# Optimization experiments

Hardware: AMD Instinct MI355X
Metric: run time of the kernel (lower is better)

Reference implementation:

```python
import jax, jax.numpy as jnp
import numpy as np

DIM = 1024
K = 3
T = 32768


def setup_inputs() -> dict:
    key = jax.random.key(0)
    k1, k2 = jax.random.split(key)
    x = jax.random.normal(k1, (T, DIM), dtype=jnp.float32)
    coeffs = jax.random.normal(k2, (DIM, 2 * K + 1), dtype=jnp.float32) * 0.001
    return {"x": x, "coeffs": coeffs}


def reference(x, coeffs):
    # coeffs layout per original module: [:, 0] constant, [:, 2k-1] sin(k*x), [:, 2k] cos(k*x)
    ks = jnp.arange(1, K + 1, dtype=x.dtype)            # [K]
    ang = x[:, :, None] * ks                            # [T, D, K]
    s = jnp.sin(ang)                                    # [T, D, K]
    c = jnp.cos(ang)                                    # [T, D, K]
    c_const = coeffs[:, 0]                              # [D]
    c_sin = coeffs[:, 1::2]                             # [D, K] (indices 1,3,5)
    c_cos = coeffs[:, 2::2]                             # [D, K] (indices 2,4,6)
    correction = (c_const[None, :]
                  + jnp.einsum('tdk,dk->td', s, c_sin)
                  + jnp.einsum('tdk,dk->td', c, c_cos))
    return x + correction
```

## Files before the change

### kernel.cpp

```cpp
#include <hip/hip_runtime.h>
#include <math.h>

#define DIM   1024
#define NROWS 32768

__global__ __launch_bounds__(256) void fourier_kan_kernel(
    const float* __restrict__ x, const float* __restrict__ coeffs,
    float* __restrict__ out, int n_rows)
{
    const int tid = threadIdx.x;
    const int d0  = tid * 4;

    float cc0[4], cs1[4], cc1[4], cs2[4], cc2[4], cs3[4], cc3[4];
#pragma unroll
    for (int j = 0; j < 4; ++j) {
        const float* cp = coeffs + (size_t)(d0 + j) * 7;
        cc0[j] = cp[0];
        cs1[j] = cp[1]; cc1[j] = cp[2];
        cs2[j] = cp[3]; cc2[j] = cp[4];
        cs3[j] = cp[5]; cc3[j] = cp[6];
    }

    for (int t = blockIdx.x; t < n_rows; t += gridDim.x) {
        const size_t base = (size_t)t * DIM + d0;
        const float4 xv = *reinterpret_cast<const float4*>(x + base);
        float xin[4] = {xv.x, xv.y, xv.z, xv.w};
        float o[4];
#pragma unroll
        for (int j = 0; j < 4; ++j) {
            float s1, c1;
            __sincosf(xin[j], &s1, &c1);
            const float s2 = 2.0f * s1 * c1;
            const float c2 = 1.0f - 2.0f * s1 * s1;
            const float s3 = s2 * c1 + c2 * s1;
            const float c3 = c2 * c1 - s2 * s1;
            float corr = cc0[j];
            corr = fmaf(s1, cs1[j], corr);
            corr = fmaf(c1, cc1[j], corr);
            corr = fmaf(s2, cs2[j], corr);
            corr = fmaf(c2, cc2[j], corr);
            corr = fmaf(s3, cs3[j], corr);
            corr = fmaf(c3, cc3[j], corr);
            o[j] = xin[j] + corr;
        }
        float4 ov = {o[0], o[1], o[2], o[3]};
        *reinterpret_cast<float4*>(out + base) = ov;
    }
}

extern "C" void kernel_launch(void* const* d_in, const int* in_sizes, int n_in,
                              void* d_out, int out_size, void* d_ws, size_t ws_size,
                              hipStream_t stream) {
    const float* x      = (const float*)d_in[0];
    const float* coeffs = (const float*)d_in[1];
    float* out          = (float*)d_out;
    (void)in_sizes; (void)n_in; (void)out_size; (void)d_ws; (void)ws_size;

    const int grid = 4096;
    fourier_kan_kernel<<<grid, 256, 0, stream>>>(x, coeffs, out, NROWS);
}
```

Measured before the change: 238.7 us.

## Issue eight row loads up front per block with vector coeff loads and nontemporal stores

Replaces the grid-stride row loop with a fixed 8 rows per block, issuing all eight float4 loads before any compute so more memory requests are in flight per thread. Coefficients are now read as seven 16-byte vector loads instead of 28 scalar loads. Output uses nontemporal stores to avoid polluting cache. The grid becomes 4096 blocks each covering exactly 8 rows, so NROWS must be a multiple of RPB.

```diff
diff --git a/kernel.cpp b/kernel.cpp
--- a/kernel.cpp
+++ b/kernel.cpp
@@ -3,49 +3,60 @@
 
 #define DIM   1024
 #define NROWS 32768
+#define RPB   8
+
+typedef float v4f __attribute__((ext_vector_type(4)));
+
+__device__ __forceinline__ float fk_elem(float xin,
+    float C0, float S1, float C1, float S2, float C2, float S3, float C3)
+{
+    float s1, c1;
+    __sincosf(xin, &s1, &c1);
+    const float s2 = 2.0f * s1 * c1;
+    const float c2 = 1.0f - 2.0f * s1 * s1;
+    const float s3 = s2 * c1 + c2 * s1;
+    const float c3 = c2 * c1 - s2 * s1;
+    float corr = C0;
+    corr = fmaf(s1, S1, corr);
+    corr = fmaf(c1, C1, corr);
+    corr = fmaf(s2, S2, corr);
+    corr = fmaf(c2, C2, corr);
+    corr = fmaf(s3, S3, corr);
+    corr = fmaf(c3, C3, corr);
+    return xin + corr;
+}
 
 __global__ __launch_bounds__(256) void fourier_kan_kernel(
     const float* __restrict__ x, const float* __restrict__ coeffs,
-    float* __restrict__ out, int n_rows)
+    float* __restrict__ out)
 {
     const int tid = threadIdx.x;
-    const int d0  = tid * 4;
+    const int t0  = blockIdx.x * RPB;
 
-    float cc0[4], cs1[4], cc1[4], cs2[4], cc2[4], cs3[4], cc3[4];
-#pragma unroll
-    for (int j = 0; j < 4; ++j) {
-        const float* cp = coeffs + (size_t)(d0 + j) * 7;
-        cc0[j] = cp[0];
-        cs1[j] = cp[1]; cc1[j] = cp[2];
-        cs2[j] = cp[3]; cc2[j] = cp[4];
-        cs3[j] = cp[5]; cc3[j] = cp[6];
-    }
+    const v4f* cp = reinterpret_cast<const v4f*>(coeffs + (size_t)tid * 28);
+    const v4f q0 = cp[0], q1 = cp[1], q2 = cp[2], q3 = cp[3],
+              q4 = cp[4], q5 = cp[5], q6 = cp[6];
 
-    for (int t = blockIdx.x; t < n_rows; t += gridDim.x) {
-        const size_t base = (size_t)t * DIM + d0;
-        const float4 xv = *reinterpret_cast<const float4*>(x + base);
-        float xin[4] = {xv.x, xv.y, xv.z, xv.w};
-        float o[4];
-#pragma unroll
-        for (int j = 0; j < 4; ++j) {
-            float s1, c1;
-            __sincosf(xin[j], &s1, &c1);
-            const float s2 = 2.0f * s1 * c1;
-            const float c2 = 1.0f - 2.0f * s1 * s1;
-            const float s3 = s2 * c1 + c2 * s1;
-            const float c3 = c2 * c1 - s2 * s1;
-            float corr = cc0[j];
-            corr = fmaf(s1, cs1[j], corr);
-            corr = fmaf(c1, cc1[j], corr);
-            corr = fmaf(s2, cs2[j], corr);
-            corr = fmaf(c2, cc2[j], corr);
-            corr = fmaf(s3, cs3[j], corr);
-            corr = fmaf(c3, cc3[j], corr);
-            o[j] = xin[j] + corr;
-        }
-        float4 ov = {o[0], o[1], o[2], o[3]};
-        *reinterpret_cast<float4*>(out + base) = ov;
-    }
+    const v4f* xr  = reinterpret_cast<const v4f*>(x + (size_t)t0 * DIM) + tid;
+    v4f*       orw = reinterpret_cast<v4f*>(out + (size_t)t0 * DIM) + tid;
+
+    const v4f x0 = xr[0 * 256], x1 = xr[1 * 256], x2 = xr[2 * 256],
+              x3 = xr[3 * 256], x4 = xr[4 * 256], x5 = xr[5 * 256],
+              x6 = xr[6 * 256], x7 = xr[7 * 256];
+
+#define FK_ROW(xv, r)                                                         \
+    do {                                                                      \
+        v4f ov;                                                               \
+        ov.x = fk_elem(xv.x, q0.x, q0.y, q0.z, q0.w, q1.x, q1.y, q1.z);       \
+        ov.y = fk_elem(xv.y, q1.w, q2.x, q2.y, q2.z, q2.w, q3.x, q3.y);       \
+        ov.z = fk_elem(xv.z, q3.z, q3.w, q4.x, q4.y, q4.z, q4.w, q5.x);       \
+        ov.w = fk_elem(xv.w, q5.y, q5.z, q5.w, q6.x, q6.y, q6.z, q6.w);       \
+        __builtin_nontemporal_store(ov, orw + (r) * 256);                     \
+    } while (0)
+
+    FK_ROW(x0, 0); FK_ROW(x1, 1); FK_ROW(x2, 2); FK_ROW(x3, 3);
+    FK_ROW(x4, 4); FK_ROW(x5, 5); FK_ROW(x6, 6); FK_ROW(x7, 7);
+#undef FK_ROW
 }
 
 extern "C" void kernel_launch(void* const* d_in, const int* in_sizes, int n_in,
@@ -56,6 +67,6 @@
     float* out          = (float*)d_out;
     (void)in_sizes; (void)n_in; (void)out_size; (void)d_ws; (void)ws_size;
 
-    const int grid = 4096;
-    fourier_kan_kernel<<<grid, 256, 0, stream>>>(x, coeffs, out, NROWS);
+    const int grid = NROWS / RPB;
+    fourier_kan_kernel<<<grid, 256, 0, stream>>>(x, coeffs, out);
 }
```

After: 232.0 us. 1.03x faster.
